# Kernel tuning notes

Hardware: AMD Instinct MI355X
Metric: run time of the kernel (lower is better)

The kernel has to match this reference:

```python
import jax, jax.numpy as jnp
import numpy as np

B, LS, LT = 64, 64, 64
E, H = 512, 512
VS, VT = 32000, 32000


def setup_inputs() -> dict:
    key = jax.random.key(0)
    ks = jax.random.split(key, 16)
    s = 0.02
    inp = {
        "src": jax.random.randint(ks[0], (B, LS), 0, VS),
        "tgt": jax.random.randint(ks[1], (B, LT), 0, VT),
        # encoder params
        "src_embed": jax.random.normal(ks[2], (VS, E), jnp.float32) * s,
        "enc_Wx": jax.random.normal(ks[3], (E, 4 * H), jnp.float32) * s,   # [i|f|g|o]
        "enc_Wh": jax.random.normal(ks[4], (H, 4 * H), jnp.float32) * s,
        "enc_b": jnp.zeros((4 * H,), jnp.float32),
        # decoder params
        "tgt_embed": jax.random.normal(ks[5], (VT, E), jnp.float32) * s,
        "att_Wh": jax.random.normal(ks[6], (H, H), jnp.float32) * s,
        "att_Ws": jax.random.normal(ks[7], (H, H), jnp.float32) * s,
        "att_v": jax.random.normal(ks[8], (H,), jnp.float32) * s,
        "dec_Wx": jax.random.normal(ks[9], (E + H, 4 * H), jnp.float32) * s,
        "dec_Wh": jax.random.normal(ks[10], (H, 4 * H), jnp.float32) * s,
        "dec_b": jnp.zeros((4 * H,), jnp.float32),
        "h2o_W": jax.random.normal(ks[11], (2 * H, VT), jnp.float32) * s,
        "h2o_b": jnp.zeros((VT,), jnp.float32),
    }
    return inp


def _lstm_step(x, h, c, Wx, Wh, b):
    # x:(B,in), h,c:(B,H). Gates packed as [i|f|g|o] along last dim (same math
    # as 8 separate nn.Linear calls with biases summed).
    z = x @ Wx + h @ Wh + b
    i, f, g, o = jnp.split(z, 4, axis=-1)
    c_new = jax.nn.sigmoid(f) * c + jax.nn.sigmoid(i) * jnp.tanh(g)
    h_new = jax.nn.sigmoid(o) * jnp.tanh(c_new)
    return h_new, c_new


def reference(src, tgt, src_embed, enc_Wx, enc_Wh, enc_b, tgt_embed,
              att_Wh, att_Ws, att_v, dec_Wx, dec_Wh, dec_b, h2o_W, h2o_b):
    Bs = src.shape[0]
    h0 = jnp.zeros((Bs, H), jnp.float32)
    c0 = jnp.zeros((Bs, H), jnp.float32)

    # ---- encoder: scan over source timesteps ----
    src_emb = src_embed[src]                       # (B,Ls,E)
    xs_enc = jnp.swapaxes(src_emb, 0, 1)           # (Ls,B,E)

    def enc_step(carry, x):
        h, c = carry
        h, c = _lstm_step(x, h, c, enc_Wx, enc_Wh, enc_b)
        return (h, c), h

    (h_enc, c_enc), enc_hs = jax.lax.scan(enc_step, (h0, c0), xs_enc)
    enc_hiddens = jnp.swapaxes(enc_hs, 0, 1)       # (B,Ls,H)

    # encoder-side attention projection is decoder-state independent: hoist it
    enc_t = enc_hiddens @ att_Wh                   # (B,Ls,H)

    # ---- decoder: teacher forcing, scan over target timesteps ----
    tgt_emb = tgt_embed[tgt]                       # (B,Lt,E)
    xs_dec = jnp.swapaxes(tgt_emb, 0, 1)           # (Lt,B,E)

    def dec_step(carry, emb):
        h, c = carry
        # Bahdanau additive attention on previous decoder hidden h
        dec_t = h @ att_Ws                                        # (B,H)
        energy = jnp.tanh(enc_t + dec_t[:, None, :]) @ att_v      # (B,Ls)
        attn = jax.nn.softmax(energy, axis=-1)                    # (B,Ls)
        context = jnp.einsum('bs,bsh->bh', attn, enc_hiddens)     # (B,H)
        lstm_in = jnp.concatenate([emb, context], axis=-1)        # (B,E+H)
        h, c = _lstm_step(lstm_in, h, c, dec_Wx, dec_Wh, dec_b)
        logits = jnp.concatenate([h, context], axis=-1) @ h2o_W + h2o_b
        out = jax.nn.log_softmax(logits, axis=-1)                 # (B,Vt)
        return (h, c), out

    _, outs = jax.lax.scan(dec_step, (h_enc, c_enc), xs_dec)      # (Lt,B,Vt)
    return jnp.swapaxes(outs, 0, 1)                               # (B,Lt,Vt)
```

## Files before the change

kernel.cpp:

```cpp
#include <hip/hip_runtime.h>
#include <hip/hip_bf16.h>
#include <math.h>

#define BB 64
#define LL 64
#define EE 512
#define HH 512
#define G4 2048
#define VT 32000
#define RT 4096

typedef unsigned short u16;
typedef unsigned int u32;
typedef __attribute__((ext_vector_type(8))) unsigned short ushort8;
typedef __attribute__((ext_vector_type(8))) short bf16x8;
typedef __attribute__((ext_vector_type(4))) float f32x4;

__device__ u16   gW2T[(size_t)VT * 1024];
__device__ u16   gEncWxT[G4 * EE];
__device__ u16   gEncWhT[G4 * HH];
__device__ u16   gAttWhT[HH * HH];
__device__ u16   gDecWxTe[G4 * EE];
__device__ u16   gDecWxTc[G4 * HH];
__device__ u16   gDecWhT[G4 * HH];
__device__ u16   gWsB[HH * HH];
__device__ u16   gSrcEmb[RT * EE];
__device__ u16   gTgtEmb[RT * EE];
__device__ float gXWxE[(size_t)RT * G4];
__device__ float gXWxD[(size_t)RT * G4];
__device__ u16   gEncHb[(size_t)RT * HH];
__device__ u16   gEncHb2[(size_t)RT * HH];
__device__ u16   gEncTb[(size_t)RT * HH];
__device__ u16   gHcat[(size_t)RT * 1024];
__device__ float gC[BB * HH];
__device__ float gAv[HH];
__device__ unsigned gFlagE[64];
__device__ unsigned gFlagB[64];
__device__ unsigned gFlagC[64];

__device__ __forceinline__ u16 f2b(float f) {
    union { float f; unsigned u; } v{f};
    unsigned r = v.u + 0x7fffu + ((v.u >> 16) & 1u);
    return (u16)(r >> 16);
}
__device__ __forceinline__ float b2f(u16 x) {
    union { unsigned u; float f; } v; v.u = ((unsigned)x) << 16; return v.f;
}
__device__ __forceinline__ float sigm(float x) { return 1.f / (1.f + __expf(-x)); }
__device__ __forceinline__ float ftanh(float x) {
    x = fminf(15.f, fmaxf(-15.f, x));
    float e = __expf(2.f * x);
    return (e - 1.f) / (e + 1.f);
}

__device__ __forceinline__ void ld16(const void* addr, bf16x8* a) {
    asm volatile(
        "global_load_dwordx4 %0, %16, off sc0 sc1\n\t"
        "global_load_dwordx4 %1, %16, off offset:64 sc0 sc1\n\t"
        "global_load_dwordx4 %2, %16, off offset:128 sc0 sc1\n\t"
        "global_load_dwordx4 %3, %16, off offset:192 sc0 sc1\n\t"
        "global_load_dwordx4 %4, %16, off offset:256 sc0 sc1\n\t"
        "global_load_dwordx4 %5, %16, off offset:320 sc0 sc1\n\t"
        "global_load_dwordx4 %6, %16, off offset:384 sc0 sc1\n\t"
        "global_load_dwordx4 %7, %16, off offset:448 sc0 sc1\n\t"
        "global_load_dwordx4 %8, %16, off offset:512 sc0 sc1\n\t"
        "global_load_dwordx4 %9, %16, off offset:576 sc0 sc1\n\t"
        "global_load_dwordx4 %10, %16, off offset:640 sc0 sc1\n\t"
        "global_load_dwordx4 %11, %16, off offset:704 sc0 sc1\n\t"
        "global_load_dwordx4 %12, %16, off offset:768 sc0 sc1\n\t"
        "global_load_dwordx4 %13, %16, off offset:832 sc0 sc1\n\t"
        "global_load_dwordx4 %14, %16, off offset:896 sc0 sc1\n\t"
        "global_load_dwordx4 %15, %16, off offset:960 sc0 sc1\n\t"
        "s_waitcnt vmcnt(0)"
        : "=&v"(a[0]), "=&v"(a[1]), "=&v"(a[2]), "=&v"(a[3]),
          "=&v"(a[4]), "=&v"(a[5]), "=&v"(a[6]), "=&v"(a[7]),
          "=&v"(a[8]), "=&v"(a[9]), "=&v"(a[10]), "=&v"(a[11]),
          "=&v"(a[12]), "=&v"(a[13]), "=&v"(a[14]), "=&v"(a[15])
        : "v"(addr) : "memory");
}
__device__ __forceinline__ u32 ld1(const void* addr) {
    u32 r;
    asm volatile("global_load_dword %0, %1, off sc0 sc1\n\ts_waitcnt vmcnt(0)"
                 : "=&v"(r) : "v"(addr) : "memory");
    return r;
}
__device__ __forceinline__ void st16b(u16* p, u16 v) {
    u32 vv = v;
    asm volatile("global_store_short %0, %1, off sc0 sc1" :: "v"(p), "v"(vv) : "memory");
}
__device__ __forceinline__ void st32b(u32* p, u32 v) {
    asm volatile("global_store_dword %0, %1, off sc0 sc1" :: "v"(p), "v"(v) : "memory");
}

__device__ __forceinline__ void setflag(unsigned* f, unsigned v) {
    asm volatile("s_waitcnt vmcnt(0)" ::: "memory");
    __syncthreads();
    if (threadIdx.x == 0) st32b((u32*)f, v);
}
__device__ __forceinline__ void waitflags(unsigned* flags, int n, unsigned target) {
    if (threadIdx.x < 64) {
        const unsigned* p = flags + (threadIdx.x & (n - 1));
        for (;;) {
            u32 v = ld1(p);
            if (__all(v >= target)) break;
            __builtin_amdgcn_s_sleep(1);
        }
    }
    __syncthreads();
}

__device__ __forceinline__ void g2l16(const u16* g, u16* l) {
    __builtin_amdgcn_global_load_lds(
        (const __attribute__((address_space(1))) unsigned int*)g,
        (__attribute__((address_space(3))) unsigned int*)l, 16, 0, 0);
}

__device__ inline u16* bf16sel(int s) {
    switch (s) {
        case 0: return gW2T;    case 1: return gEncWxT; case 2: return gEncWhT;
        case 3: return gAttWhT; case 4: return gDecWxTe; case 5: return gDecWxTc;
        default: return gDecWhT;
    }
}

__global__ __launch_bounds__(256) void k_transpose(const float* __restrict__ in, int R, int C, int sel) {
    __shared__ float tile[32][33];
    int tx = threadIdx.x & 31, ty0 = threadIdx.x >> 5;
    int c0 = blockIdx.x * 32, r0 = blockIdx.y * 32;
#pragma unroll
    for (int k = 0; k < 4; k++) {
        int ty = ty0 + k * 8;
        tile[ty][tx] = in[(size_t)(r0 + ty) * C + c0 + tx];
    }
    __syncthreads();
    u16* out = bf16sel(sel);
#pragma unroll
    for (int k = 0; k < 4; k++) {
        int ty = ty0 + k * 8;
        out[(size_t)(c0 + ty) * R + r0 + tx] = f2b(tile[tx][ty]);
    }
}

__global__ __launch_bounds__(256) void k_tobf(const float* __restrict__ in) {
    int i = blockIdx.x * 256 + threadIdx.x;
    gWsB[i] = f2b(in[i]);
}

__global__ __launch_bounds__(256) void k_gather(const int* __restrict__ tok, const float* __restrict__ tab, int sel) {
    int r = blockIdx.x;
    int b = r & 63, t = r >> 6;
    int token = tok[b * LL + t];
    u16* dst = (sel == 0) ? gSrcEmb : gTgtEmb;
    const float* srow = tab + (size_t)token * EE;
    for (int e = threadIdx.x; e < EE; e += 256)
        dst[(size_t)r * EE + e] = f2b(srow[e]);
}

__global__ __launch_bounds__(256) void k_zero() {
    int i = blockIdx.x * 256 + threadIdx.x;
    gC[i] = 0.f;
    if (i < 64) st32b((u32*)(gFlagE + i), 0u);
}

__global__ __launch_bounds__(256) void k_rst(const float* __restrict__ av) {
    int t = threadIdx.x;
    gAv[t] = av[t];
    gAv[t + 256] = av[t + 256];
    if (t < 64) {
        st32b((u32*)(gFlagB + t), 0u);
        st32b((u32*)(gFlagC + t), 0u);
    }
}

__global__ __launch_bounds__(256) void k_gemm(int selA, int lda, int selB, int ldb,
                                              int M, int N, int K, int epi,
                                              const float* __restrict__ bias, int selOut) {
    __shared__ u16 sA[128 * 72];
    __shared__ u16 sB[128 * 72];
    const u16* Ag;
    switch (selA) { case 0: Ag = gSrcEmb; break; case 1: Ag = gTgtEmb; break; default: Ag = gEncHb; }
    const u16* Bg;
    switch (selB) { case 0: Bg = gEncWxT; break; case 1: Bg = gDecWxTe; break; default: Bg = gAttWhT; }
    float* Cg = (selOut == 0) ? gXWxE : gXWxD;

    int tid = threadIdx.x, l = tid & 63, wid = tid >> 6, wr = wid >> 1, wc = wid & 1;
    int ar = l & 15, ak = (l >> 4) * 8;
    int rowM = blockIdx.y * 128, colN = blockIdx.x * 128;
    f32x4 acc[4][4];
#pragma unroll
    for (int m = 0; m < 4; m++)
#pragma unroll
        for (int n = 0; n < 4; n++) acc[m][n] = (f32x4){0.f, 0.f, 0.f, 0.f};

    for (int k0 = 0; k0 < K; k0 += 64) {
#pragma unroll
        for (int it = 0; it < 4; it++) {
            int idx = it * 256 + tid;
            int row = idx >> 3, cc = idx & 7;
            *(ushort8*)(sA + row * 72 + cc * 8) =
                *(const ushort8*)(Ag + (size_t)(rowM + row) * lda + k0 + cc * 8);
            *(ushort8*)(sB + row * 72 + cc * 8) =
                *(const ushort8*)(Bg + (size_t)(colN + row) * ldb + k0 + cc * 8);
        }
        __syncthreads();
#pragma unroll
        for (int ks = 0; ks < 2; ks++) {
            bf16x8 a[4], b[4];
#pragma unroll
            for (int m = 0; m < 4; m++) a[m] = *(const bf16x8*)(sA + (wr * 64 + m * 16 + ar) * 72 + ks * 32 + ak);
#pragma unroll
            for (int n = 0; n < 4; n++) b[n] = *(const bf16x8*)(sB + (wc * 64 + n * 16 + ar) * 72 + ks * 32 + ak);
#pragma unroll
            for (int m = 0; m < 4; m++)
#pragma unroll
                for (int n = 0; n < 4; n++)
                    acc[m][n] = __builtin_amdgcn_mfma_f32_16x16x32_bf16(a[m], b[n], acc[m][n], 0, 0, 0);
        }
        __syncthreads();
    }
    int rb = (l >> 4) * 4;
#pragma unroll
    for (int m = 0; m < 4; m++)
#pragma unroll
        for (int n = 0; n < 4; n++)
#pragma unroll
            for (int ri = 0; ri < 4; ri++) {
                int row = rowM + wr * 64 + m * 16 + rb + ri;
                int col = colN + wc * 64 + n * 16 + ar;
                float v = acc[m][n][ri];
                if (epi == 2) Cg[(size_t)row * N + col] = v + bias[col];
                else gEncTb[(size_t)((row & 63) * 64 + (row >> 6)) * N + col] = f2b(v);
            }
}

__global__ __launch_bounds__(256) void k_gemm_big(const float* __restrict__ bias, float* __restrict__ out) {
    __shared__ u16 sA[128 * 64];
    __shared__ u16 sB[128 * 64];
    int tid = threadIdx.x, l = tid & 63, wid = tid >> 6, wr = wid >> 1, wc = wid & 1;
    int ar = l & 15, ak = (l >> 4) * 8, rb = (l >> 4) * 4;
    int bid = (blockIdx.x & 7) * 1000 + (blockIdx.x >> 3);
    int bxx = bid % (VT / 128), byy = bid / (VT / 128);
    int rowM = byy * 128, colN = bxx * 128;
    f32x4 acc[4][4];
#pragma unroll
    for (int m = 0; m < 4; m++)
#pragma unroll
        for (int n = 0; n < 4; n++) acc[m][n] = (f32x4){0.f, 0.f, 0.f, 0.f};

    int srow = wid * 32 + (l >> 3);
    int scol = (l & 7) * 8;
    for (int k0 = 0; k0 < 1024; k0 += 64) {
#pragma unroll
        for (int c = 0; c < 4; c++) {
            int r = srow + c * 8;
            g2l16(gHcat + (size_t)(rowM + r) * 1024 + k0 + scol, sA + r * 64 + scol);
            g2l16(gW2T + (size_t)(colN + r) * 1024 + k0 + scol, sB + r * 64 + scol);
        }
        __syncthreads();
#pragma unroll
        for (int ks = 0; ks < 2; ks++) {
            bf16x8 a[4], b[4];
#pragma unroll
            for (int m = 0; m < 4; m++) a[m] = *(const bf16x8*)(sA + (wr * 64 + m * 16 + ar) * 64 + ks * 32 + ak);
#pragma unroll
            for (int n = 0; n < 4; n++) b[n] = *(const bf16x8*)(sB + (wc * 64 + n * 16 + ar) * 64 + ks * 32 + ak);
#pragma unroll
            for (int m = 0; m < 4; m++)
#pragma unroll
                for (int n = 0; n < 4; n++)
                    acc[m][n] = __builtin_amdgcn_mfma_f32_16x16x32_bf16(a[m], b[n], acc[m][n], 0, 0, 0);
        }
        __syncthreads();
    }
#pragma unroll
    for (int m = 0; m < 4; m++)
#pragma unroll
        for (int n = 0; n < 4; n++)
#pragma unroll
            for (int ri = 0; ri < 4; ri++) {
                int row = rowM + wr * 64 + m * 16 + rb + ri;
                int col = colN + wc * 64 + n * 16 + ar;
                out[(size_t)((row & 63) * 64 + (row >> 6)) * VT + col] = acc[m][n][ri] + bias[col];
            }
}

__global__ __launch_bounds__(256) void k_encoder(int dummy) {
    __shared__ u16 sW[64 * 512];
    int tid = threadIdx.x, l = tid & 63, wid = tid >> 6;
    int j = blockIdx.x;
#pragma unroll
    for (int it = 0; it < 16; it++) {
        int idx = it * 256 + tid;
        int lr = idx >> 6, kc = idx & 63;
        int gcol = (lr >> 4) * 512 + j * 16 + (lr & 15);
        int off = (lr * 1024 + kc * 16) ^ ((lr & 7) << 4);
        *(ushort8*)((char*)sW + off) = *(const ushort8*)(gEncWhT + (size_t)gcol * 512 + kc * 8);
    }
    __syncthreads();
    int ar = l & 15, ak = (l >> 4) * 8, rb = (l >> 4) * 4;
    int arow = wid * 16 + ar, aoff = (l >> 4) * 16;
    for (int t = 0; t < LL; t++) {
        f32x4 acc[4];
#pragma unroll
        for (int g = 0; g < 4; g++) acc[g] = (f32x4){0.f, 0.f, 0.f, 0.f};
        if (t > 0) {
            waitflags(gFlagE, 32, (unsigned)t);
            bf16x8 af[16];
            ld16((const char*)gEncHb + (size_t)((t - 1) * BB + arow) * 1024 + aoff, af);
#pragma unroll
            for (int kk = 0; kk < 16; kk++) {
                int k = kk * 32 + ak;
#pragma unroll
                for (int g = 0; g < 4; g++) {
                    int lr = g * 16 + ar;
                    bf16x8 b = *(const bf16x8*)((char*)sW + ((lr * 1024 + k * 2) ^ ((lr & 7) << 4)));
                    acc[g] = __builtin_amdgcn_mfma_f32_16x16x32_bf16(af[kk], b, acc[g], 0, 0, 0);
                }
            }
        }
        int hcol = j * 16 + ar;
#pragma unroll
        for (int ri = 0; ri < 4; ri++) {
            int row = wid * 16 + rb + ri;
            int rr = t * BB + row;
            const float* xw = gXWxE + (size_t)rr * G4;
            float zi = acc[0][ri] + xw[hcol];
            float zf = acc[1][ri] + xw[512 + hcol];
            float zg = acc[2][ri] + xw[1024 + hcol];
            float zo = acc[3][ri] + xw[1536 + hcol];
            float co = gC[row * HH + hcol];
            float cn = sigm(zf) * co + sigm(zi) * ftanh(zg);
            float hn = sigm(zo) * ftanh(cn);
            gC[row * HH + hcol] = cn;
            u16 hb = f2b(hn);
            st16b(gEncHb + (size_t)rr * HH + hcol, hb);
            gEncHb2[(size_t)(row * LL + t) * HH + hcol] = hb;
        }
        setflag(gFlagE + j, (unsigned)(t + 1));
    }
}

__global__ __launch_bounds__(256) void k_decoder(int dummy) {
    __shared__ u16 sWh[64 * 512];
    __shared__ u16 sWx[64 * 512];
    __shared__ float s_h[512];
    __shared__ float s_dt[512];
    __shared__ float s_av[512];
    __shared__ float s_att[64];
    __shared__ float s_red[256];
    __shared__ float s_mv[4][520];
    int tid = threadIdx.x, l = tid & 63, wid = tid >> 6;
    int bx = blockIdx.x;
    int ar = l & 15, ak = (l >> 4) * 8, rb = (l >> 4) * 4;
    int arow = wid * 16 + ar, aoff = (l >> 4) * 16;
    if (bx >= 64) {
        int j = bx - 64;
#pragma unroll
        for (int it = 0; it < 16; it++) {
            int idx = it * 256 + tid;
            int lr = idx >> 6, kc = idx & 63;
            int gcol = (lr >> 4) * 512 + j * 16 + (lr & 15);
            int off = (lr * 1024 + kc * 16) ^ ((lr & 7) << 4);
            *(ushort8*)((char*)sWh + off) = *(const ushort8*)(gDecWhT + (size_t)gcol * 512 + kc * 8);
            *(ushort8*)((char*)sWx + off) = *(const ushort8*)(gDecWxTc + (size_t)gcol * 512 + kc * 8);
        }
    } else {
        s_av[tid] = gAv[tid];
        s_av[tid + 256] = gAv[tid + 256];
    }
    __syncthreads();
    for (int t = 0; t < LL; t++) {
        if (bx >= 64) {
            int j = bx - 64;
            if (t > 0) waitflags(gFlagC, 32, (unsigned)t);
            bf16x8 af[16];
            const char* baseA = (t == 0)
                ? ((const char*)gEncHb + (size_t)(63 * BB + arow) * 1024 + aoff)
                : ((const char*)gHcat + (size_t)((t - 1) * BB + arow) * 2048 + aoff);
            ld16(baseA, af);
            f32x4 acc[4];
#pragma unroll
            for (int g = 0; g < 4; g++) acc[g] = (f32x4){0.f, 0.f, 0.f, 0.f};
#pragma unroll
            for (int kk = 0; kk < 16; kk++) {
                int k = kk * 32 + ak;
#pragma unroll
                for (int g = 0; g < 4; g++) {
                    int lr = g * 16 + ar;
                    bf16x8 b = *(const bf16x8*)((char*)sWh + ((lr * 1024 + k * 2) ^ ((lr & 7) << 4)));
                    acc[g] = __builtin_amdgcn_mfma_f32_16x16x32_bf16(af[kk], b, acc[g], 0, 0, 0);
                }
            }
            waitflags(gFlagB, 64, (unsigned)(t + 1));
            bf16x8 cf[16];
            ld16((const char*)gHcat + (size_t)(t * BB + arow) * 2048 + 1024 + aoff, cf);
#pragma unroll
            for (int kk = 0; kk < 16; kk++) {
                int k = kk * 32 + ak;
#pragma unroll
                for (int g = 0; g < 4; g++) {
                    int lr = g * 16 + ar;
                    bf16x8 b = *(const bf16x8*)((char*)sWx + ((lr * 1024 + k * 2) ^ ((lr & 7) << 4)));
                    acc[g] = __builtin_amdgcn_mfma_f32_16x16x32_bf16(cf[kk], b, acc[g], 0, 0, 0);
                }
            }
            int hcol = j * 16 + ar;
#pragma unroll
            for (int ri = 0; ri < 4; ri++) {
                int row = wid * 16 + rb + ri;
                int rr = t * BB + row;
                const float* xw = gXWxD + (size_t)rr * G4;
                float zi = acc[0][ri] + xw[hcol];
                float zf = acc[1][ri] + xw[512 + hcol];
                float zg = acc[2][ri] + xw[1024 + hcol];
                float zo = acc[3][ri] + xw[1536 + hcol];
                float co = gC[row * HH + hcol];
                float cn = sigm(zf) * co + sigm(zi) * ftanh(zg);
                float hn = sigm(zo) * ftanh(cn);
                gC[row * HH + hcol] = cn;
                st16b(gHcat + (size_t)rr * 1024 + hcol, f2b(hn));
            }
            setflag(gFlagC + j, (unsigned)(t + 1));
        } else {
            int b = bx;
            if (t > 0) waitflags(gFlagC, 32, (unsigned)t);
            const char* hb = (t == 0) ? ((const char*)gEncHb + (size_t)(63 * BB + b) * 1024)
                                      : ((const char*)gHcat + (size_t)((t - 1) * BB + b) * 2048);
            u32 hw = ld1(hb + 4 * tid);
            s_h[2 * tid] = b2f((u16)(hw & 0xffff));
            s_h[2 * tid + 1] = b2f((u16)(hw >> 16));
            __syncthreads();
            {
                int c8 = tid & 63, kq = tid >> 6;
                float a8[8];
#pragma unroll
                for (int jj = 0; jj < 8; jj++) a8[jj] = 0.f;
                const u16* wp = gWsB + (size_t)(kq * 128) * 512 + c8 * 8;
#pragma unroll 4
                for (int i = 0; i < 128; i++) {
                    ushort8 w = *(const ushort8*)(wp + (size_t)i * 512);
                    float hk = s_h[kq * 128 + i];
#pragma unroll
                    for (int jj = 0; jj < 8; jj++) a8[jj] += hk * b2f((u16)w[jj]);
                }
#pragma unroll
                for (int jj = 0; jj < 8; jj++) s_mv[kq][c8 * 8 + jj] = a8[jj];
            }
            __syncthreads();
            s_dt[tid] = s_mv[0][tid] + s_mv[1][tid] + s_mv[2][tid] + s_mv[3][tid];
            s_dt[tid + 256] = s_mv[0][tid + 256] + s_mv[1][tid + 256] + s_mv[2][tid + 256] + s_mv[3][tid + 256];
            __syncthreads();
            {
                int s = tid >> 2, q = tid & 3;
                const u16* et = gEncTb + (size_t)(b * 64 + s) * 512 + q * 128;
                const float* dtp = s_dt + q * 128;
                const float* avp = s_av + q * 128;
                float p = 0.f;
#pragma unroll
                for (int i = 0; i < 16; i++) {
                    ushort8 ev = *(const ushort8*)(et + i * 8);
#pragma unroll
                    for (int jj = 0; jj < 8; jj++) {
                        int h = i * 8 + jj;
                        p += ftanh(b2f((u16)ev[jj]) + dtp[h]) * avp[h];
                    }
                }
                s_red[tid] = p;
            }
            __syncthreads();
            if (tid < 64) {
                float v = s_red[tid * 4] + s_red[tid * 4 + 1] + s_red[tid * 4 + 2] + s_red[tid * 4 + 3];
                float m = v;
                for (int o = 32; o; o >>= 1) m = fmaxf(m, __shfl_xor(m, o));
                float e = __expf(v - m);
                float ss = e;
                for (int o = 32; o; o >>= 1) ss += __shfl_xor(ss, o);
                s_att[tid] = e / ss;
            }
            __syncthreads();
            int c = tid * 2;
            float c0 = 0.f, c1 = 0.f;
            const u16* eh = gEncHb2 + (size_t)b * LL * HH;
#pragma unroll 8
            for (int s2 = 0; s2 < 64; s2++) {
                float a = s_att[s2];
                u32 w = *(const u32*)(eh + (size_t)s2 * HH + c);
                c0 += a * b2f((u16)(w & 0xffff));
                c1 += a * b2f((u16)(w >> 16));
            }
            u32 cw = (u32)f2b(c0) | ((u32)f2b(c1) << 16);
            st32b((u32*)(gHcat + (size_t)(t * BB + b) * 1024 + 512 + c), cw);
            setflag(gFlagB + b, (unsigned)(t + 1));
        }
    }
}

__global__ __launch_bounds__(256) void k_lsm(float* __restrict__ out) {
    int row = blockIdx.x, tid = threadIdx.x;
    float4* p4 = (float4*)(out + (size_t)row * VT);
    float m = -1e30f, s = 0.f;
    for (int i = tid; i < VT / 4; i += 256) {
        float4 v = p4[i];
        float mx = fmaxf(fmaxf(v.x, v.y), fmaxf(v.z, v.w));
        float mn = fmaxf(m, mx);
        s = s * __expf(m - mn) + __expf(v.x - mn) + __expf(v.y - mn) + __expf(v.z - mn) + __expf(v.w - mn);
        m = mn;
    }
    for (int o = 32; o; o >>= 1) {
        float m2 = __shfl_xor(m, o), s2 = __shfl_xor(s, o);
        float mn = fmaxf(m, m2);
        s = s * __expf(m - mn) + s2 * __expf(m2 - mn);
        m = mn;
    }
    __shared__ float rm[4], rs[4];
    if ((tid & 63) == 0) { rm[tid >> 6] = m; rs[tid >> 6] = s; }
    __syncthreads();
    float mm = fmaxf(fmaxf(rm[0], rm[1]), fmaxf(rm[2], rm[3]));
    float ss = rs[0] * __expf(rm[0] - mm) + rs[1] * __expf(rm[1] - mm) +
               rs[2] * __expf(rm[2] - mm) + rs[3] * __expf(rm[3] - mm);
    float lse = mm + __logf(ss);
    for (int i = tid; i < VT / 4; i += 256) {
        float4 v = p4[i];
        v.x -= lse; v.y -= lse; v.z -= lse; v.w -= lse;
        p4[i] = v;
    }
}

extern "C" void kernel_launch(void* const* d_in, const int* in_sizes, int n_in,
                              void* d_out, int out_size, void* d_ws, size_t ws_size,
                              hipStream_t stream) {
    const int*   src       = (const int*)d_in[0];
    const int*   tgt       = (const int*)d_in[1];
    const float* src_embed = (const float*)d_in[2];
    const float* enc_Wx    = (const float*)d_in[3];
    const float* enc_Wh    = (const float*)d_in[4];
    const float* enc_b     = (const float*)d_in[5];
    const float* tgt_embed = (const float*)d_in[6];
    const float* att_Wh    = (const float*)d_in[7];
    const float* att_Ws    = (const float*)d_in[8];
    const float* att_v     = (const float*)d_in[9];
    const float* dec_Wx    = (const float*)d_in[10];
    const float* dec_Wh    = (const float*)d_in[11];
    const float* dec_b     = (const float*)d_in[12];
    const float* h2o_W     = (const float*)d_in[13];
    const float* h2o_b     = (const float*)d_in[14];
    float* out = (float*)d_out;
    dim3 blk(256);

    k_transpose<<<dim3(VT / 32, 1024 / 32), blk, 0, stream>>>(h2o_W, 1024, VT, 0);
    k_transpose<<<dim3(G4 / 32, EE / 32), blk, 0, stream>>>(enc_Wx, EE, G4, 1);
    k_transpose<<<dim3(G4 / 32, HH / 32), blk, 0, stream>>>(enc_Wh, HH, G4, 2);
    k_transpose<<<dim3(HH / 32, HH / 32), blk, 0, stream>>>(att_Wh, HH, HH, 3);
    k_transpose<<<dim3(G4 / 32, EE / 32), blk, 0, stream>>>(dec_Wx, EE, G4, 4);
    k_transpose<<<dim3(G4 / 32, HH / 32), blk, 0, stream>>>(dec_Wx + (size_t)512 * G4, HH, G4, 5);
    k_transpose<<<dim3(G4 / 32, HH / 32), blk, 0, stream>>>(dec_Wh, HH, G4, 6);
    k_tobf<<<HH * HH / 256, blk, 0, stream>>>(att_Ws);
    k_gather<<<RT, blk, 0, stream>>>(src, src_embed, 0);
    k_gather<<<RT, blk, 0, stream>>>(tgt, tgt_embed, 1);
    k_zero<<<128, blk, 0, stream>>>();
    k_gemm<<<dim3(G4 / 128, RT / 128), blk, 0, stream>>>(0, 512, 0, 512, RT, G4, 512, 2, enc_b, 0);
    k_gemm<<<dim3(G4 / 128, RT / 128), blk, 0, stream>>>(1, 512, 1, 512, RT, G4, 512, 2, dec_b, 1);
    int dummy = 0;
    void* eargs[] = { &dummy };
    hipLaunchCooperativeKernel((const void*)k_encoder, dim3(32), dim3(256), eargs, 0, stream);
    k_gemm<<<dim3(HH / 128, RT / 128), blk, 0, stream>>>(2, 512, 2, 512, RT, HH, 512, 4, nullptr, 2);
    k_rst<<<1, blk, 0, stream>>>(att_v);
    hipLaunchCooperativeKernel((const void*)k_decoder, dim3(96), dim3(256), eargs, 0, stream);
    k_gemm_big<<<(VT / 128) * (RT / 128), blk, 0, stream>>>(h2o_b, out);
    k_lsm<<<RT, blk, 0, stream>>>(out);
}
```

Baseline: 3.134 ms.

## Fuse vocab projection GEMM into cooperative decoder kernel, overlapping with recurrence

Removes the separate large h2o GEMM launch and adds 160 extra blocks to the cooperative decoder kernel. These blocks compute 128x128 output tiles as soon as flags show the needed decoder timesteps are done. The aim is to hide the serial decoder recurrence behind the large output GEMM. In exchange the extra blocks share the GPU with the latency-critical recurrence blocks and spin-wait on flags. It also relies on all 256 blocks being co-resident.

```diff
diff --git a/kernel.cpp b/kernel.cpp
--- a/kernel.cpp
+++ b/kernel.cpp
@@ -233,57 +233,6 @@
             }
 }
 
-__global__ __launch_bounds__(256) void k_gemm_big(const float* __restrict__ bias, float* __restrict__ out) {
-    __shared__ u16 sA[128 * 64];
-    __shared__ u16 sB[128 * 64];
-    int tid = threadIdx.x, l = tid & 63, wid = tid >> 6, wr = wid >> 1, wc = wid & 1;
-    int ar = l & 15, ak = (l >> 4) * 8, rb = (l >> 4) * 4;
-    int bid = (blockIdx.x & 7) * 1000 + (blockIdx.x >> 3);
-    int bxx = bid % (VT / 128), byy = bid / (VT / 128);
-    int rowM = byy * 128, colN = bxx * 128;
-    f32x4 acc[4][4];
-#pragma unroll
-    for (int m = 0; m < 4; m++)
-#pragma unroll
-        for (int n = 0; n < 4; n++) acc[m][n] = (f32x4){0.f, 0.f, 0.f, 0.f};
-
-    int srow = wid * 32 + (l >> 3);
-    int scol = (l & 7) * 8;
-    for (int k0 = 0; k0 < 1024; k0 += 64) {
-#pragma unroll
-        for (int c = 0; c < 4; c++) {
-            int r = srow + c * 8;
-            g2l16(gHcat + (size_t)(rowM + r) * 1024 + k0 + scol, sA + r * 64 + scol);
-            g2l16(gW2T + (size_t)(colN + r) * 1024 + k0 + scol, sB + r * 64 + scol);
-        }
-        __syncthreads();
-#pragma unroll
-        for (int ks = 0; ks < 2; ks++) {
-            bf16x8 a[4], b[4];
-#pragma unroll
-            for (int m = 0; m < 4; m++) a[m] = *(const bf16x8*)(sA + (wr * 64 + m * 16 + ar) * 64 + ks * 32 + ak);
-#pragma unroll
-            for (int n = 0; n < 4; n++) b[n] = *(const bf16x8*)(sB + (wc * 64 + n * 16 + ar) * 64 + ks * 32 + ak);
-#pragma unroll
-            for (int m = 0; m < 4; m++)
-#pragma unroll
-                for (int n = 0; n < 4; n++)
-                    acc[m][n] = __builtin_amdgcn_mfma_f32_16x16x32_bf16(a[m], b[n], acc[m][n], 0, 0, 0);
-        }
-        __syncthreads();
-    }
-#pragma unroll
-    for (int m = 0; m < 4; m++)
-#pragma unroll
-        for (int n = 0; n < 4; n++)
-#pragma unroll
-            for (int ri = 0; ri < 4; ri++) {
-                int row = rowM + wr * 64 + m * 16 + rb + ri;
-                int col = colN + wc * 64 + n * 16 + ar;
-                out[(size_t)((row & 63) * 64 + (row >> 6)) * VT + col] = acc[m][n][ri] + bias[col];
-            }
-}
-
 __global__ __launch_bounds__(256) void k_encoder(int dummy) {
     __shared__ u16 sW[64 * 512];
     int tid = threadIdx.x, l = tid & 63, wid = tid >> 6;
@@ -340,7 +289,8 @@
     }
 }
 
-__global__ __launch_bounds__(256) void k_decoder(int dummy) {
+__global__ __launch_bounds__(256) void k_decoder(const float* __restrict__ h2o_b,
+                                                 float* __restrict__ out) {
     __shared__ u16 sWh[64 * 512];
     __shared__ u16 sWx[64 * 512];
     __shared__ float s_h[512];
@@ -353,6 +303,61 @@
     int bx = blockIdx.x;
     int ar = l & 15, ak = (l >> 4) * 8, rb = (l >> 4) * 4;
     int arow = wid * 16 + ar, aoff = (l >> 4) * 16;
+    if (bx >= 96) {
+        u16* csA = sWh;
+        u16* csB = sWh + 128 * 64;
+        int wr = wid >> 1, wc = wid & 1;
+        int srow = wid * 32 + (l >> 3);
+        int scol = (l & 7) * 8;
+        int ci = bx - 96;
+        for (int jt = 0; jt < 50; jt++) {
+            int T = ci + 160 * jt;
+            int byy = T / 250, bxx = T % 250;
+            unsigned tgt = (unsigned)(2 * byy + 2);
+            waitflags(gFlagC, 32, tgt);
+            waitflags(gFlagB, 64, tgt);
+            int rowM = byy * 128, colN = bxx * 128;
+            f32x4 acc[4][4];
+#pragma unroll
+            for (int m = 0; m < 4; m++)
+#pragma unroll
+                for (int n = 0; n < 4; n++) acc[m][n] = (f32x4){0.f, 0.f, 0.f, 0.f};
+            for (int k0 = 0; k0 < 1024; k0 += 64) {
+#pragma unroll
+                for (int c = 0; c < 4; c++) {
+                    int r = srow + c * 8;
+                    g2l16(gHcat + (size_t)(rowM + r) * 1024 + k0 + scol, csA + r * 64 + scol);
+                    g2l16(gW2T + (size_t)(colN + r) * 1024 + k0 + scol, csB + r * 64 + scol);
+                }
+                __syncthreads();
+#pragma unroll
+                for (int ks = 0; ks < 2; ks++) {
+                    bf16x8 a[4], b[4];
+#pragma unroll
+                    for (int m = 0; m < 4; m++) a[m] = *(const bf16x8*)(csA + (wr * 64 + m * 16 + ar) * 64 + ks * 32 + ak);
+#pragma unroll
+                    for (int n = 0; n < 4; n++) b[n] = *(const bf16x8*)(csB + (wc * 64 + n * 16 + ar) * 64 + ks * 32 + ak);
+#pragma unroll
+                    for (int m = 0; m < 4; m++)
+#pragma unroll
+                        for (int n = 0; n < 4; n++)
+                            acc[m][n] = __builtin_amdgcn_mfma_f32_16x16x32_bf16(a[m], b[n], acc[m][n], 0, 0, 0);
+                }
+                __syncthreads();
+            }
+#pragma unroll
+            for (int m = 0; m < 4; m++)
+#pragma unroll
+                for (int n = 0; n < 4; n++)
+#pragma unroll
+                    for (int ri = 0; ri < 4; ri++) {
+                        int row = rowM + wr * 64 + m * 16 + rb + ri;
+                        int col = colN + wc * 64 + n * 16 + ar;
+                        out[(size_t)((row & 63) * 64 + (row >> 6)) * VT + col] = acc[m][n][ri] + h2o_b[col];
+                    }
+        }
+        return;
+    }
     if (bx >= 64) {
         int j = bx - 64;
 #pragma unroll
@@ -565,7 +570,9 @@
     hipLaunchCooperativeKernel((const void*)k_encoder, dim3(32), dim3(256), eargs, 0, stream);
     k_gemm<<<dim3(HH / 128, RT / 128), blk, 0, stream>>>(2, 512, 2, 512, RT, HH, 512, 4, nullptr, 2);
     k_rst<<<1, blk, 0, stream>>>(att_v);
-    hipLaunchCooperativeKernel((const void*)k_decoder, dim3(96), dim3(256), eargs, 0, stream);
-    k_gemm_big<<<(VT / 128) * (RT / 128), blk, 0, stream>>>(h2o_b, out);
+    const float* h2ob = h2o_b;
+    float* outp = out;
+    void* dargs[] = { (void*)&h2ob, (void*)&outp };
+    hipLaunchCooperativeKernel((const void*)k_decoder, dim3(256), dim3(256), dargs, 0, stream);
     k_lsm<<<RT, blk, 0, stream>>>(out);
 }
```

Result: no change. 3.153 ms (+0.6%).
